# Optimization experiments

Measured on AMD Instinct MI355X. Metric: run time of the kernel, lower is better.

The kernel has to match this reference:

```python
import jax, jax.numpy as jnp
import numpy as np

TEMPERATURE = 0.07


def setup_inputs() -> dict:
    key = jax.random.key(0)
    k1, k2 = jax.random.split(key)
    B, V, D = 4096, 5, 512
    img = jax.random.normal(k1, (B, D), dtype=jnp.float32)
    txt = jax.random.normal(k2, (B, V, D), dtype=jnp.float32)
    # module assumes pre-normalized features
    img = img / jnp.linalg.norm(img, axis=-1, keepdims=True)
    txt = txt / jnp.linalg.norm(txt, axis=-1, keepdims=True)
    return {"image_features": img, "text_features_all": txt}


def reference(image_features, text_features_all):
    B, V, D = text_features_all.shape
    text_flat = text_features_all.reshape(B * V, D)          # (BV, D)
    logits = (image_features @ text_flat.T) / TEMPERATURE    # (B, BV)

    # i2t: per image-row, soft targets = 1/V on its V positive texts
    row_lse = jax.nn.logsumexp(logits, axis=1)               # (B,)
    pos_logits = logits.reshape(B, B, V)[jnp.arange(B), jnp.arange(B)]  # (B, V)
    loss_i2t = jnp.mean(row_lse - jnp.mean(pos_logits, axis=1))

    # t2i: per text-column, cross-entropy over B images, target = col // V
    col_lse = jax.nn.logsumexp(logits, axis=0)               # (BV,)
    img_idx = jnp.arange(B * V) // V
    pos_col = logits[img_idx, jnp.arange(B * V)]             # (BV,)
    loss_t2i = jnp.mean(col_lse - pos_col)

    return (loss_i2t + loss_t2i) * 0.5
```

## Files before the change

### kernel.cpp

```cpp
#include <hip/hip_runtime.h>
#include <stdint.h>

#define B_  4096
#define V_  5
#define D_  512
#define NN_ (B_ * V_)
#define NBLK_ 5120
#define NIMG4_ ((B_ * D_) / 4)

#define C_EXP 20.609929155556620f
#define M_SHIFT (1.0f / 0.07f)
#define SCALE1 0x7f7f7f7f

typedef float floatx4 __attribute__((ext_vector_type(4)));
typedef int   intx4   __attribute__((ext_vector_type(4)));
typedef int   intx8   __attribute__((ext_vector_type(8)));

__device__ __forceinline__ void load_lds16(const void* g, void* l) {
  __builtin_amdgcn_global_load_lds(
      (const __attribute__((address_space(1))) unsigned int*)g,
      (__attribute__((address_space(3))) unsigned int*)l,
      16, 0, 0);
}

template <int CTRL>
__device__ __forceinline__ float dppadd(float v) {
  int r = __builtin_amdgcn_update_dpp(0, __builtin_bit_cast(int, v),
                                      CTRL, 0xF, 0xF, true);
  return v + __builtin_bit_cast(float, r);
}
__device__ __forceinline__ float sum16(float v) {
  v = dppadd<0x128>(v);
  v = dppadd<0x124>(v);
  v = dppadd<0x122>(v);
  v = dppadd<0x121>(v);
  return v;
}

__global__ void cvt_kernel(const float* __restrict__ img, const float* __restrict__ txt,
                           uint32_t* __restrict__ out32, float* __restrict__ acc) {
  const int tid0 = blockIdx.x * 256 + threadIdx.x;
  if (tid0 < B_ + NN_) acc[tid0] = 0.0f;
#pragma unroll
  for (int it = 0; it < 4; ++it) {
    const int idx = tid0 + it * (3072 * 256);
    float4 v = (idx < NIMG4_) ? ((const float4*)img)[idx]
                              : ((const float4*)txt)[idx - NIMG4_];
    int w = __builtin_amdgcn_cvt_pk_fp8_f32(v.x, v.y, 0, 0);
    w     = __builtin_amdgcn_cvt_pk_fp8_f32(v.z, v.w, w, 1);
    out32[idx] = (uint32_t)w;
  }
}

__global__ __launch_bounds__(256, 4)
void gemm_kernel(const uint8_t* __restrict__ Ah, const uint8_t* __restrict__ Bh,
                 float* __restrict__ row_sum, float* __restrict__ col_sum,
                 float* __restrict__ posPart) {
  __shared__ __align__(16) uint8_t As[2 * 128 * 64];
  __shared__ __align__(16) uint8_t Bs[2 * 128 * 64];
  const int tid  = threadIdx.x;
  const int lane = tid & 63;
  const int w    = tid >> 6;
  const int wm   = w >> 1, wn = w & 1;
  const int m0   = blockIdx.x * 128;
  const int n0   = blockIdx.y * 128;

  floatx4 acc[4][4] = {};

  const int sc = ((lane & 3) ^ ((lane >> 3) & 3)) * 16;
  const uint8_t* gA = Ah + (size_t)(m0 + w * 32 + (lane >> 2)) * D_ + sc;
  const uint8_t* gB = Bh + (size_t)(n0 + w * 32 + (lane >> 2)) * D_ + sc;
  const int lofs = (w * 32) * 64;

  const int fr  = lane & 15;
  const int swz = (fr >> 1) & 3;
  const int qb  = (lane >> 5) & 1;
  const int qh  = (lane >> 4) & 1;
  const int c0  = ((qh * 2 + 0) ^ swz) * 16;
  const int c1  = ((qh * 2 + 1) ^ swz) * 16;
  const int bufo = qb * 8192;

  #define STAGE(s) do {                                            \
    const int kg = (s) * 128;                                      \
    load_lds16(gA + kg,                As + lofs);                 \
    load_lds16(gA + kg + 16 * D_,      As + lofs + 16 * 64);       \
    load_lds16(gB + kg,                Bs + lofs);                 \
    load_lds16(gB + kg + 16 * D_,      Bs + lofs + 16 * 64);       \
    load_lds16(gA + kg + 64,           As + 8192 + lofs);          \
    load_lds16(gA + kg + 64 + 16 * D_, As + 8192 + lofs + 16 * 64);\
    load_lds16(gB + kg + 64,           Bs + 8192 + lofs);          \
    load_lds16(gB + kg + 64 + 16 * D_, Bs + 8192 + lofs + 16 * 64);\
  } while (0)

  STAGE(0);

#pragma unroll
  for (int ss = 0; ss < 4; ++ss) {
    __syncthreads();

    intx8 af[4], bf[4];
#pragma unroll
    for (int f = 0; f < 4; ++f) {
      const uint8_t* Ar = As + bufo + (wm * 64 + f * 16 + fr) * 64;
      const uint8_t* Br = Bs + bufo + (wn * 64 + f * 16 + fr) * 64;
      intx4 alo = *(const intx4*)(Ar + c0);
      intx4 ahi = *(const intx4*)(Ar + c1);
      intx4 blo = *(const intx4*)(Br + c0);
      intx4 bhi = *(const intx4*)(Br + c1);
      af[f] = __builtin_shufflevector(alo, ahi, 0, 1, 2, 3, 4, 5, 6, 7);
      bf[f] = __builtin_shufflevector(blo, bhi, 0, 1, 2, 3, 4, 5, 6, 7);
    }

    __syncthreads();

    if (ss < 3) STAGE(ss + 1);

#pragma unroll
    for (int mf = 0; mf < 4; ++mf)
#pragma unroll
      for (int nf = 0; nf < 4; ++nf)
        acc[mf][nf] = __builtin_amdgcn_mfma_scale_f32_16x16x128_f8f6f4(
            af[mf], bf[nf], acc[mf][nf],
            0, 0,
            0, SCALE1,
            0, SCALE1);
  }
  #undef STAGE

  {
    float ps = 0.0f;
    const int iLo = n0 / 5, iHi = (n0 + 127) / 5;
    if (iHi >= m0 && iLo < m0 + 128) {
      const int rbase = m0 + wm * 64 + ((lane >> 4) << 2);
#pragma unroll
      for (int nf = 0; nf < 4; ++nf) {
        const int ci = (n0 + wn * 64 + nf * 16 + (lane & 15)) / 5;
#pragma unroll
        for (int mf = 0; mf < 4; ++mf)
#pragma unroll
          for (int r = 0; r < 4; ++r)
            if (rbase + mf * 16 + r == ci) ps += acc[mf][nf][r];
      }
    }
    ps = sum16(ps);
    ps += __shfl_xor(ps, 16);
    ps += __shfl_xor(ps, 32);
    __shared__ float pls[4];
    if (lane == 0) pls[w] = ps;
    __syncthreads();
    if (tid == 0)
      posPart[blockIdx.y * 32 + blockIdx.x] = pls[0] + pls[1] + pls[2] + pls[3];
  }

#pragma unroll
  for (int mf = 0; mf < 4; ++mf)
#pragma unroll
    for (int nf = 0; nf < 4; ++nf)
#pragma unroll
      for (int r = 0; r < 4; ++r)
        acc[mf][nf][r] = exp2f(acc[mf][nf][r] * C_EXP - C_EXP);

  float cs[4];
#pragma unroll
  for (int nf = 0; nf < 4; ++nf) {
    float s = 0.0f;
#pragma unroll
    for (int mf = 0; mf < 4; ++mf)
      s += acc[mf][nf][0] + acc[mf][nf][1] + acc[mf][nf][2] + acc[mf][nf][3];
    s += __shfl_xor(s, 16);
    s += __shfl_xor(s, 32);
    cs[nf] = s;
  }
  {
    int g = lane >> 4;
    float v = (g == 0) ? cs[0] : (g == 1) ? cs[1] : (g == 2) ? cs[2] : cs[3];
    atomicAdd(&col_sum[n0 + wn * 64 + (g << 4) + (lane & 15)], v);
  }

#pragma unroll
  for (int mf = 0; mf < 4; ++mf) {
    floatx4 t = acc[mf][0] + acc[mf][1] + acc[mf][2] + acc[mf][3];
#pragma unroll
    for (int r = 0; r < 4; ++r) t[r] = sum16(t[r]);
    if ((lane & 15) < 4) {
      int q = lane & 3;
      float v = (q == 0) ? t[0] : (q == 1) ? t[1] : (q == 2) ? t[2] : t[3];
      atomicAdd(&row_sum[m0 + wm * 64 + mf * 16 + ((lane >> 4) << 2) + q], v);
    }
  }
}

__global__ void finish_kernel(const float* __restrict__ acc, const float* __restrict__ posPart,
                              float* __restrict__ out) {
  int tid = threadIdx.x;
  float sA = 0.0f, sB = 0.0f, sP = 0.0f;
  for (int i = tid; i < B_;    i += 1024) sA += logf(acc[i]);
  for (int i = tid; i < NN_;   i += 1024) sB += logf(acc[B_ + i]);
  for (int i = tid; i < NBLK_; i += 1024) sP += posPart[i];
  float s = sA * (1.0f / B_) + sB * (1.0f / NN_)
          - sP * (2.0f * M_SHIFT / (float)NN_);
  for (int o = 32; o; o >>= 1) s += __shfl_xor(s, o);
  __shared__ float ls[16];
  int lane = tid & 63, w = tid >> 6;
  if (lane == 0) ls[w] = s;
  __syncthreads();
  if (tid == 0) {
    float tot = 0.0f;
#pragma unroll
    for (int i = 0; i < 16; ++i) tot += ls[i];
    out[0] = M_SHIFT + 0.5f * tot;
  }
}

extern "C" void kernel_launch(void* const* d_in, const int* in_sizes, int n_in,
                              void* d_out, int out_size, void* d_ws, size_t ws_size,
                              hipStream_t stream) {
  const float* img = (const float*)d_in[0];
  const float* txt = (const float*)d_in[1];

  const size_t fp8Bytes = (size_t)(B_ * D_ + NN_ * D_);
  const size_t needBytes = fp8Bytes + (size_t)(B_ + NN_ + NBLK_) * 4;
  if (ws_size < needBytes) return;

  uint8_t* Ah  = (uint8_t*)d_ws;
  uint8_t* Bh  = Ah + (size_t)B_ * D_;
  float* acc   = (float*)((char*)d_ws + fp8Bytes);
  float* row_s = acc;
  float* col_s = acc + B_;
  float* posP  = acc + B_ + NN_;

  cvt_kernel   <<<3072, 256, 0, stream>>>(img, txt, (uint32_t*)Ah, acc);
  gemm_kernel  <<<dim3(32, 160), 256, 0, stream>>>(Ah, Bh, row_s, col_s, posP);
  finish_kernel<<<1, 1024, 0, stream>>>(acc, posP, (float*)d_out);
}
```

Baseline: 150.9 us.

## Parallelize finish reduction across blocks, raise MFMA wave priority, use union fragments

The final reduction kernel now runs on 16 blocks instead of one, and each block atomically adds its partial to the output. The output is pre-initialized to the constant shift inside the convert kernel. The GEMM main loop raises wave priority around the MFMA burst, and A/B fragments are built through a union instead of a shufflevector. The multi-block finish removes a serial single-block tail, but it makes the result depend on floating-point atomic ordering.

```diff
diff --git a/kernel.cpp b/kernel.cpp
--- a/kernel.cpp
+++ b/kernel.cpp
@@ -12,6 +12,8 @@
 #define M_SHIFT (1.0f / 0.07f)
 #define SCALE1 0x7f7f7f7f
 
+#define FIN_BLOCKS 16
+
 typedef float floatx4 __attribute__((ext_vector_type(4)));
 typedef int   intx4   __attribute__((ext_vector_type(4)));
 typedef int   intx8   __attribute__((ext_vector_type(8)));
@@ -38,9 +40,11 @@
 }
 
 __global__ void cvt_kernel(const float* __restrict__ img, const float* __restrict__ txt,
-                           uint32_t* __restrict__ out32, float* __restrict__ acc) {
+                           uint32_t* __restrict__ out32, float* __restrict__ acc,
+                           float* __restrict__ out) {
   const int tid0 = blockIdx.x * 256 + threadIdx.x;
   if (tid0 < B_ + NN_) acc[tid0] = 0.0f;
+  if (tid0 == 0) out[0] = M_SHIFT;
 #pragma unroll
   for (int it = 0; it < 4; ++it) {
     const int idx = tid0 + it * (3072 * 256);
@@ -51,6 +55,8 @@
     out32[idx] = (uint32_t)w;
   }
 }
+
+union V8 { intx8 v8; intx4 v4[2]; };
 
 __global__ __launch_bounds__(256, 4)
 void gemm_kernel(const uint8_t* __restrict__ Ah, const uint8_t* __restrict__ Bh,
@@ -98,32 +104,32 @@
   for (int ss = 0; ss < 4; ++ss) {
     __syncthreads();
 
-    intx8 af[4], bf[4];
+    V8 af[4], bf[4];
 #pragma unroll
     for (int f = 0; f < 4; ++f) {
       const uint8_t* Ar = As + bufo + (wm * 64 + f * 16 + fr) * 64;
       const uint8_t* Br = Bs + bufo + (wn * 64 + f * 16 + fr) * 64;
-      intx4 alo = *(const intx4*)(Ar + c0);
-      intx4 ahi = *(const intx4*)(Ar + c1);
-      intx4 blo = *(const intx4*)(Br + c0);
-      intx4 bhi = *(const intx4*)(Br + c1);
-      af[f] = __builtin_shufflevector(alo, ahi, 0, 1, 2, 3, 4, 5, 6, 7);
-      bf[f] = __builtin_shufflevector(blo, bhi, 0, 1, 2, 3, 4, 5, 6, 7);
+      af[f].v4[0] = *(const intx4*)(Ar + c0);
+      af[f].v4[1] = *(const intx4*)(Ar + c1);
+      bf[f].v4[0] = *(const intx4*)(Br + c0);
+      bf[f].v4[1] = *(const intx4*)(Br + c1);
     }
 
     __syncthreads();
 
     if (ss < 3) STAGE(ss + 1);
 
+    __builtin_amdgcn_s_setprio(1);
 #pragma unroll
     for (int mf = 0; mf < 4; ++mf)
 #pragma unroll
       for (int nf = 0; nf < 4; ++nf)
         acc[mf][nf] = __builtin_amdgcn_mfma_scale_f32_16x16x128_f8f6f4(
-            af[mf], bf[nf], acc[mf][nf],
+            af[mf].v8, bf[nf].v8, acc[mf][nf],
             0, 0,
             0, SCALE1,
             0, SCALE1);
+    __builtin_amdgcn_s_setprio(0);
   }
   #undef STAGE
 
@@ -192,23 +198,24 @@
 
 __global__ void finish_kernel(const float* __restrict__ acc, const float* __restrict__ posPart,
                               float* __restrict__ out) {
-  int tid = threadIdx.x;
+  const int tid = blockIdx.x * 1024 + threadIdx.x;
+  const int stride = FIN_BLOCKS * 1024;
   float sA = 0.0f, sB = 0.0f, sP = 0.0f;
-  for (int i = tid; i < B_;    i += 1024) sA += logf(acc[i]);
-  for (int i = tid; i < NN_;   i += 1024) sB += logf(acc[B_ + i]);
-  for (int i = tid; i < NBLK_; i += 1024) sP += posPart[i];
+  for (int i = tid; i < B_;    i += stride) sA += logf(acc[i]);
+  for (int i = tid; i < NN_;   i += stride) sB += logf(acc[B_ + i]);
+  for (int i = tid; i < NBLK_; i += stride) sP += posPart[i];
   float s = sA * (1.0f / B_) + sB * (1.0f / NN_)
           - sP * (2.0f * M_SHIFT / (float)NN_);
   for (int o = 32; o; o >>= 1) s += __shfl_xor(s, o);
   __shared__ float ls[16];
-  int lane = tid & 63, w = tid >> 6;
+  int lane = threadIdx.x & 63, w = threadIdx.x >> 6;
   if (lane == 0) ls[w] = s;
   __syncthreads();
-  if (tid == 0) {
+  if (threadIdx.x == 0) {
     float tot = 0.0f;
 #pragma unroll
     for (int i = 0; i < 16; ++i) tot += ls[i];
-    out[0] = M_SHIFT + 0.5f * tot;
+    atomicAdd(out, 0.5f * tot);
   }
 }
 
@@ -229,7 +236,7 @@
   float* col_s = acc + B_;
   float* posP  = acc + B_ + NN_;
 
-  cvt_kernel   <<<3072, 256, 0, stream>>>(img, txt, (uint32_t*)Ah, acc);
+  cvt_kernel   <<<3072, 256, 0, stream>>>(img, txt, (uint32_t*)Ah, acc, (float*)d_out);
   gemm_kernel  <<<dim3(32, 160), 256, 0, stream>>>(Ah, Bh, row_s, col_s, posP);
-  finish_kernel<<<1, 1024, 0, stream>>>(acc, posP, (float*)d_out);
-}
+  finish_kernel<<<FIN_BLOCKS, 1024, 0, stream>>>(acc, posP, (float*)d_out);
+}
```

Measured after the change: 254.1 us. 68.3% more time.
